# Kernel optimization log

Measured on AMD Instinct MI355X. Metric: run time of the kernel, lower is better.

The kernel has to match this reference:

```python
import jax, jax.numpy as jnp
import numpy as np

N = 100000   # nodes
E = 1600000  # edges (avg degree 16)
F = 128      # num_features
H = 128      # hidden_channels
C = 8        # num_classes


def _gcn_conv(x, src, dst, W, b, num_nodes):
    """PyG GCNConv: add self-loops, symmetric normalization, linear-then-aggregate, +bias."""
    h = x @ W  # [N, out]
    loops = jnp.arange(num_nodes, dtype=src.dtype)
    s = jnp.concatenate([src, loops])
    d = jnp.concatenate([dst, loops])
    deg = jax.ops.segment_sum(jnp.ones_like(s, dtype=h.dtype), d, num_segments=num_nodes)
    dinv = jax.lax.rsqrt(jnp.maximum(deg, 1.0))  # deg >= 1 thanks to self-loops
    norm = dinv[s] * dinv[d]  # [E+N]
    out = jax.ops.segment_sum(h[s] * norm[:, None], d, num_segments=num_nodes)
    return out + b


def setup_inputs() -> dict:
    key = jax.random.key(0)
    k1, k2, k3, k4 = jax.random.split(key, 4)
    x = jax.random.normal(k1, (N, F), dtype=jnp.float32)
    edge_index = jax.random.randint(k2, (2, E), 0, N, dtype=jnp.int32)
    W1 = jax.random.normal(k3, (F, H), dtype=jnp.float32) * (1.0 / np.sqrt(F))
    b1 = jnp.zeros((H,), dtype=jnp.float32)
    W2 = jax.random.normal(k4, (H, C), dtype=jnp.float32) * (1.0 / np.sqrt(H))
    b2 = jnp.zeros((C,), dtype=jnp.float32)
    return {"x": x, "edge_index": edge_index, "W1": W1, "b1": b1, "W2": W2, "b2": b2}


def reference(x, edge_index, W1, b1, W2, b2):
    src, dst = edge_index[0], edge_index[1]
    h = _gcn_conv(x, src, dst, W1, b1, N)
    h = jax.nn.relu(h)
    out = _gcn_conv(h, src, dst, W2, b2, N)
    return out
```

## Files before the change

### kernel.cpp

```cpp
#include <hip/hip_runtime.h>
#include <hip/hip_bf16.h>
#include <hip/hip_fp16.h>

#define NN 100000
#define EE 1600000
#define FF 128
#define HH 128
#define CC 8

#define CH 4096
#define NBK ((NN + 255) / 256)
#define NCH ((EE + CH - 1) / CH)
#define HSZ (NBK * NCH)

typedef _Float16 half8 __attribute__((ext_vector_type(8)));
typedef float f32x4 __attribute__((ext_vector_type(4)));

__global__ __launch_bounds__(1024) void k_scan1(const int* __restrict__ in,
                                                int* __restrict__ outp,
                                                int* __restrict__ bsum, int n) {
  __shared__ int sh[1024];
  int t = threadIdx.x;
  int i = blockIdx.x * 1024 + t;
  int v = (i < n) ? in[i] : 0;
  sh[t] = v;
  __syncthreads();
  for (int offs = 1; offs < 1024; offs <<= 1) {
    int add = (t >= offs) ? sh[t - offs] : 0;
    __syncthreads();
    sh[t] += add;
    __syncthreads();
  }
  if (i < n) outp[i] = sh[t] - v;
  if (t == 1023) bsum[blockIdx.x] = sh[1023];
}

__global__ __launch_bounds__(256) void k_scan2(int* __restrict__ bsum, int nb) {
  __shared__ int sh[256];
  int t = threadIdx.x;
  int v = (t < nb) ? bsum[t] : 0;
  sh[t] = v;
  __syncthreads();
  for (int offs = 1; offs < 256; offs <<= 1) {
    int add = (t >= offs) ? sh[t - offs] : 0;
    __syncthreads();
    sh[t] += add;
    __syncthreads();
  }
  if (t < nb) bsum[t] = sh[t] - v;
}

__global__ __launch_bounds__(1024) void k_scan3(int* __restrict__ outp,
                                                const int* __restrict__ bsum,
                                                int n, int e) {
  int i = blockIdx.x * 1024 + threadIdx.x;
  if (i < n) outp[i] += bsum[blockIdx.x];
  if (i == 0) outp[n] = e;
}

__global__ __launch_bounds__(256) void k_histA(const int* __restrict__ dst,
                                               int* __restrict__ hist) {
  __shared__ int lh[NBK];
  int c = blockIdx.x, t = threadIdx.x;
  for (int b = t; b < NBK; b += 256) lh[b] = 0;
  __syncthreads();
  int e0 = c * CH, e1 = min(e0 + CH, EE);
  for (int j = e0 + t; j < e1; j += 256) atomicAdd(&lh[dst[j] >> 8], 1);
  __syncthreads();
  for (int b = t; b < NBK; b += 256) hist[b * NCH + c] = lh[b];
}

__global__ __launch_bounds__(256) void k_scat_gemm1(
    const int* __restrict__ src, const int* __restrict__ dst,
    const int* __restrict__ hoff, unsigned int* __restrict__ stage,
    const float* __restrict__ x, const float* __restrict__ W,
    __half* __restrict__ h, int n) {
  __shared__ _Float16 Wl[128 * 128];
  int t = threadIdx.x;

  if (blockIdx.x < NCH) {
    int* lcur = (int*)Wl;
    int c = blockIdx.x;
    for (int b = t; b < NBK; b += 256) lcur[b] = hoff[b * NCH + c];
    __syncthreads();
    int e0 = c * CH, e1 = min(e0 + CH, EE);
    for (int j = e0 + t; j < e1; j += 256) {
      int d = dst[j];
      int pos = atomicAdd(&lcur[d >> 8], 1);
      stage[pos] = (unsigned int)src[j] | ((unsigned int)(d & 255) << 17);
    }
    return;
  }

  {
    int c = t & 127;
    int kg0 = t >> 7;
    for (int kg = kg0; kg < 16; kg += 2) {
      _Float16 tmp[8];
#pragma unroll
      for (int j = 0; j < 8; ++j)
        tmp[j] = (_Float16)W[(size_t)(kg * 8 + j) * 128 + c];
      int byteoff = (c * 256 + kg * 16) ^ ((c & 7) << 4);
      *(half8*)((char*)Wl + byteoff) = *(half8*)tmp;
    }
  }
  __syncthreads();

  int row0 = (blockIdx.x - NCH) * 64;
  int w = t >> 6, l = t & 63;
  int rw = w >> 1, cw = w & 1;
  int lr = l & 15, g = l >> 4;

  f32x4 acc[2][4];
#pragma unroll
  for (int ar = 0; ar < 2; ++ar)
#pragma unroll
    for (int bt = 0; bt < 4; ++bt)
#pragma unroll
      for (int r = 0; r < 4; ++r) acc[ar][bt][r] = 0.f;

  for (int kt = 0; kt < 4; ++kt) {
    half8 a[2];
#pragma unroll
    for (int ar = 0; ar < 2; ++ar) {
      int row = row0 + rw * 32 + ar * 16 + lr;
      if (row < n) {
        const float* p = &x[(size_t)row * 128 + kt * 32 + g * 8];
        float4 v0 = *(const float4*)p;
        float4 v1 = *(const float4*)(p + 4);
        a[ar][0] = (_Float16)v0.x; a[ar][1] = (_Float16)v0.y;
        a[ar][2] = (_Float16)v0.z; a[ar][3] = (_Float16)v0.w;
        a[ar][4] = (_Float16)v1.x; a[ar][5] = (_Float16)v1.y;
        a[ar][6] = (_Float16)v1.z; a[ar][7] = (_Float16)v1.w;
      } else {
#pragma unroll
        for (int j = 0; j < 8; ++j) a[ar][j] = (_Float16)0.f;
      }
    }
#pragma unroll
    for (int bt = 0; bt < 4; ++bt) {
      int c = cw * 64 + bt * 16 + lr;
      int byteoff = (c * 256 + kt * 64 + g * 16) ^ ((c & 7) << 4);
      half8 bb = *(const half8*)((const char*)Wl + byteoff);
      acc[0][bt] = __builtin_amdgcn_mfma_f32_16x16x32_f16(a[0], bb, acc[0][bt], 0, 0, 0);
      acc[1][bt] = __builtin_amdgcn_mfma_f32_16x16x32_f16(a[1], bb, acc[1][bt], 0, 0, 0);
    }
  }

#pragma unroll
  for (int ar = 0; ar < 2; ++ar)
#pragma unroll
    for (int bt = 0; bt < 4; ++bt)
#pragma unroll
      for (int r = 0; r < 4; ++r) {
        int row = row0 + rw * 32 + ar * 16 + g * 4 + r;
        int c = cw * 64 + bt * 16 + lr;
        if (row < n) h[(size_t)row * 128 + c] = __float2half(acc[ar][bt][r]);
      }
}

__global__ __launch_bounds__(256) void k_bucketB(const unsigned int* __restrict__ stage,
                                                 const int* __restrict__ hoff,
                                                 int* __restrict__ col,
                                                 int* __restrict__ rowptr,
                                                 float* __restrict__ dinv) {
  __shared__ int lcnt[256];
  __shared__ int lpart[256];
  int b = blockIdx.x, t = threadIdx.x;
  int n0 = b * 256;
  lcnt[t] = 0;
  __syncthreads();
  int e0 = hoff[b * NCH];
  int e1 = hoff[(b + 1) * NCH];
  for (int j = e0 + t; j < e1; j += 256)
    atomicAdd(&lcnt[stage[j] >> 17], 1);
  __syncthreads();
  int c = lcnt[t];
  lpart[t] = c;
  __syncthreads();
  for (int offs = 1; offs < 256; offs <<= 1) {
    int add = (t >= offs) ? lpart[t - offs] : 0;
    __syncthreads();
    lpart[t] += add;
    __syncthreads();
  }
  int base = e0 + lpart[t] - c;
  int node = n0 + t;
  if (node <= NN) rowptr[node] = base;
  if (node < NN) dinv[node] = rsqrtf((float)c + 1.f);
  __syncthreads();
  lcnt[t] = base;
  __syncthreads();
  for (int j = e0 + t; j < e1; j += 256) {
    unsigned int v = stage[j];
    int pos = atomicAdd(&lcnt[v >> 17], 1);
    col[pos] = (int)(v & 0x1FFFFu);
  }
}

__global__ __launch_bounds__(256) void k_agg1(const __half* __restrict__ h,
                                              const int* __restrict__ rowptr,
                                              const int* __restrict__ col,
                                              const float* __restrict__ dinv,
                                              const float* __restrict__ b1,
                                              __half2* __restrict__ out, int n) {
  int wid = threadIdx.x >> 6;
  int lane = threadIdx.x & 63;
  int node = blockIdx.x * 4 + wid;
  if (node >= n) return;
  float dn = dinv[node];
  const __half2* hp = (const __half2*)h;
  float2 acc = make_float2(0.f, 0.f);
  int e0 = rowptr[node], e1 = rowptr[node + 1];
  int e = e0;
  for (; e + 7 < e1; e += 8) {
    int s[8];
#pragma unroll
    for (int u = 0; u < 8; ++u) s[u] = col[e + u];
    float w[8];
    __half2 f[8];
#pragma unroll
    for (int u = 0; u < 8; ++u) w[u] = dinv[s[u]];
#pragma unroll
    for (int u = 0; u < 8; ++u) f[u] = hp[(size_t)s[u] * 64 + lane];
#pragma unroll
    for (int u = 0; u < 8; ++u) {
      float2 ff = __half22float2(f[u]);
      float ww = w[u] * dn;
      acc.x = fmaf(ww, ff.x, acc.x);
      acc.y = fmaf(ww, ff.y, acc.y);
    }
  }
  for (; e + 1 < e1; e += 2) {
    int s0 = col[e], s1 = col[e + 1];
    float w0 = dinv[s0] * dn, w1 = dinv[s1] * dn;
    float2 f0 = __half22float2(hp[(size_t)s0 * 64 + lane]);
    float2 f1 = __half22float2(hp[(size_t)s1 * 64 + lane]);
    acc.x = fmaf(w0, f0.x, acc.x); acc.y = fmaf(w0, f0.y, acc.y);
    acc.x = fmaf(w1, f1.x, acc.x); acc.y = fmaf(w1, f1.y, acc.y);
  }
  if (e < e1) {
    int s = col[e];
    float w = dinv[s] * dn;
    float2 f = __half22float2(hp[(size_t)s * 64 + lane]);
    acc.x = fmaf(w, f.x, acc.x);
    acc.y = fmaf(w, f.y, acc.y);
  }
  {
    float w = dn * dn;
    float2 f = __half22float2(hp[(size_t)node * 64 + lane]);
    acc.x = fmaf(w, f.x, acc.x);
    acc.y = fmaf(w, f.y, acc.y);
  }
  float2 bb = ((const float2*)b1)[lane];
  acc.x = fmaxf(acc.x + bb.x, 0.f);
  acc.y = fmaxf(acc.y + bb.y, 0.f);
  out[(size_t)node * 64 + lane] = __floats2half2_rn(acc.x, acc.y);
}

__global__ __launch_bounds__(256) void k_gemm2(const __half* __restrict__ a,
                                               const float* __restrict__ W2,
                                               __half* __restrict__ h2, int n) {
  int r = blockIdx.x * 256 + threadIdx.x;
  if (r >= n) return;
  float acc[8];
#pragma unroll
  for (int c = 0; c < 8; ++c) acc[c] = 0.f;
  const __half2* ap = (const __half2*)(a + (size_t)r * 128);
#pragma unroll 8
  for (int k2 = 0; k2 < 64; ++k2) {
    float2 v = __half22float2(ap[k2]);
    int k = k2 * 2;
#pragma unroll
    for (int c = 0; c < 8; ++c) {
      acc[c] = fmaf(v.x, W2[(k + 0) * 8 + c], acc[c]);
      acc[c] = fmaf(v.y, W2[(k + 1) * 8 + c], acc[c]);
    }
  }
  union { __half2 h2v[4]; uint4 u; } pk;
#pragma unroll
  for (int c = 0; c < 4; ++c)
    pk.h2v[c] = __floats2half2_rn(acc[2 * c], acc[2 * c + 1]);
  *(uint4*)&h2[(size_t)r * 8] = pk.u;
}

__global__ __launch_bounds__(256) void k_agg2(const __half* __restrict__ h2,
                                              const int* __restrict__ rowptr,
                                              const int* __restrict__ col,
                                              const float* __restrict__ dinv,
                                              const float* __restrict__ b2,
                                              float* __restrict__ out, int n) {
  int gthread = blockIdx.x * 256 + threadIdx.x;
  int node = gthread >> 3, f = gthread & 7;
  if (node >= n) return;
  float dn = dinv[node];
  float acc = 0.f;
  int e0 = rowptr[node], e1 = rowptr[node + 1];
  int e = e0;
  for (; e + 3 < e1; e += 4) {
    int s0 = col[e], s1 = col[e + 1], s2 = col[e + 2], s3 = col[e + 3];
    float w0 = dinv[s0], w1 = dinv[s1], w2 = dinv[s2], w3 = dinv[s3];
    float v0 = __half2float(h2[(size_t)s0 * 8 + f]);
    float v1 = __half2float(h2[(size_t)s1 * 8 + f]);
    float v2 = __half2float(h2[(size_t)s2 * 8 + f]);
    float v3 = __half2float(h2[(size_t)s3 * 8 + f]);
    acc = fmaf(w0 * dn, v0, acc);
    acc = fmaf(w1 * dn, v1, acc);
    acc = fmaf(w2 * dn, v2, acc);
    acc = fmaf(w3 * dn, v3, acc);
  }
  for (; e < e1; ++e) {
    int s = col[e];
    acc = fmaf(dinv[s] * dn, __half2float(h2[(size_t)s * 8 + f]), acc);
  }
  acc = fmaf(dn * dn, __half2float(h2[(size_t)node * 8 + f]), acc);
  out[(size_t)node * 8 + f] = acc + b2[f];
}

extern "C" void kernel_launch(void* const* d_in, const int* in_sizes, int n_in,
                              void* d_out, int out_size, void* d_ws, size_t ws_size,
                              hipStream_t stream) {
  const float* x  = (const float*)d_in[0];
  const int* eidx = (const int*)d_in[1];
  const float* W1 = (const float*)d_in[2];
  const float* b1 = (const float*)d_in[3];
  const float* W2 = (const float*)d_in[4];
  const float* b2 = (const float*)d_in[5];
  float* out = (float*)d_out;
  const int* src = eidx;
  const int* dst = eidx + EE;

  char* ws = (char*)d_ws;
  size_t off = 0;
  auto alloc = [&](size_t bytes) -> char* {
    char* p = ws + off;
    off = (off + bytes + 255) & ~(size_t)255;
    return p;
  };

  float*        dinv   = (float*)       alloc((size_t)NN * 4);
  int*          rowptr = (int*)         alloc((size_t)(NN + 1) * 4);
  int*          bsum   = (int*)         alloc(1024 * 4);
  int*          hist_g = (int*)         alloc((size_t)HSZ * 4);
  int*          hist_s = (int*)         alloc((size_t)(HSZ + 1) * 4);
  unsigned int* stage  = (unsigned int*)alloc((size_t)EE * 4);
  int*          colbuf = (int*)         alloc((size_t)EE * 4);
  __half*       h1     = (__half*)      alloc((size_t)NN * HH * 2);
  __half2*      agg1   = (__half2*)     alloc((size_t)NN * HH * 2);
  __half*       h2     = (__half*)h1;

  int nbScanH = (HSZ + 1023) / 1024;

  k_histA<<<NCH, 256, 0, stream>>>(dst, hist_g);
  k_scan1<<<nbScanH, 1024, 0, stream>>>(hist_g, hist_s, bsum, HSZ);
  k_scan2<<<1, 256, 0, stream>>>(bsum, nbScanH);
  k_scan3<<<nbScanH, 1024, 0, stream>>>(hist_s, bsum, HSZ, EE);

  int nbG1 = (NN + 63) / 64;
  k_scat_gemm1<<<NCH + nbG1, 256, 0, stream>>>(src, dst, hist_s, stage,
                                               x, W1, h1, NN);
  k_bucketB<<<NBK, 256, 0, stream>>>(stage, hist_s, colbuf, rowptr, dinv);

  k_agg1<<<(NN + 3) / 4, 256, 0, stream>>>(h1, rowptr, colbuf, dinv, b1, agg1, NN);
  k_gemm2<<<(NN + 255) / 256, 256, 0, stream>>>((const __half*)agg1, W2, h2, NN);
  k_agg2<<<(NN * 8 + 255) / 256, 256, 0, stream>>>(h2, rowptr, colbuf, dinv,
                                                   b2, out, NN);
}
```

Measured before the change: 165.9 us.

## Fold scan fixup into consumers, stage buckets in LDS, deepen gather unrolls

Drops the k_scan3 launch by having the scatter and bucket kernels add the block-level scan offsets themselves. It doubles the edge chunk size, which halves the histogram size. k_bucketB now copies each bucket's staged edges into shared memory so the second pass avoids re-reading global memory, and falls back to the old path when a bucket holds more than BCAP edges. The gather loops in agg1 and agg2 are unrolled further to keep more loads in flight, at the cost of more registers and possibly lower occupancy.

```diff
diff --git a/kernel.cpp b/kernel.cpp
--- a/kernel.cpp
+++ b/kernel.cpp
@@ -8,10 +8,11 @@
 #define HH 128
 #define CC 8
 
-#define CH 4096
+#define CH 8192
 #define NBK ((NN + 255) / 256)
 #define NCH ((EE + CH - 1) / CH)
 #define HSZ (NBK * NCH)
+#define BCAP 6144
 
 typedef _Float16 half8 __attribute__((ext_vector_type(8)));
 typedef float f32x4 __attribute__((ext_vector_type(4)));
@@ -50,14 +51,6 @@
   if (t < nb) bsum[t] = sh[t] - v;
 }
 
-__global__ __launch_bounds__(1024) void k_scan3(int* __restrict__ outp,
-                                                const int* __restrict__ bsum,
-                                                int n, int e) {
-  int i = blockIdx.x * 1024 + threadIdx.x;
-  if (i < n) outp[i] += bsum[blockIdx.x];
-  if (i == 0) outp[n] = e;
-}
-
 __global__ __launch_bounds__(256) void k_histA(const int* __restrict__ dst,
                                                int* __restrict__ hist) {
   __shared__ int lh[NBK];
@@ -72,7 +65,8 @@
 
 __global__ __launch_bounds__(256) void k_scat_gemm1(
     const int* __restrict__ src, const int* __restrict__ dst,
-    const int* __restrict__ hoff, unsigned int* __restrict__ stage,
+    const int* __restrict__ hist_s, const int* __restrict__ bsum,
+    unsigned int* __restrict__ stage,
     const float* __restrict__ x, const float* __restrict__ W,
     __half* __restrict__ h, int n) {
   __shared__ _Float16 Wl[128 * 128];
@@ -81,7 +75,10 @@
   if (blockIdx.x < NCH) {
     int* lcur = (int*)Wl;
     int c = blockIdx.x;
-    for (int b = t; b < NBK; b += 256) lcur[b] = hoff[b * NCH + c];
+    for (int b = t; b < NBK; b += 256) {
+      int idx = b * NCH + c;
+      lcur[b] = hist_s[idx] + bsum[idx >> 10];
+    }
     __syncthreads();
     int e0 = c * CH, e1 = min(e0 + CH, EE);
     for (int j = e0 + t; j < e1; j += 256) {
@@ -160,20 +157,38 @@
 }
 
 __global__ __launch_bounds__(256) void k_bucketB(const unsigned int* __restrict__ stage,
-                                                 const int* __restrict__ hoff,
+                                                 const int* __restrict__ hist_s,
+                                                 const int* __restrict__ bsum,
                                                  int* __restrict__ col,
                                                  int* __restrict__ rowptr,
                                                  float* __restrict__ dinv) {
+  __shared__ unsigned int sstage[BCAP];
   __shared__ int lcnt[256];
   __shared__ int lpart[256];
   int b = blockIdx.x, t = threadIdx.x;
   int n0 = b * 256;
   lcnt[t] = 0;
-  __syncthreads();
-  int e0 = hoff[b * NCH];
-  int e1 = hoff[(b + 1) * NCH];
-  for (int j = e0 + t; j < e1; j += 256)
-    atomicAdd(&lcnt[stage[j] >> 17], 1);
+  int i0 = b * NCH;
+  int e0 = hist_s[i0] + bsum[i0 >> 10];
+  int e1;
+  if (b == NBK - 1) {
+    e1 = EE;
+  } else {
+    int i1 = (b + 1) * NCH;
+    e1 = hist_s[i1] + bsum[i1 >> 10];
+  }
+  int cnt = e1 - e0;
+  bool lds_path = (cnt <= BCAP);
+  __syncthreads();
+  if (lds_path) {
+    for (int j = t; j < cnt; j += 256) {
+      unsigned int v = stage[e0 + j];
+      sstage[j] = v;
+      atomicAdd(&lcnt[v >> 17], 1);
+    }
+  } else {
+    for (int j = e0 + t; j < e1; j += 256) atomicAdd(&lcnt[stage[j] >> 17], 1);
+  }
   __syncthreads();
   int c = lcnt[t];
   lpart[t] = c;
@@ -191,10 +206,18 @@
   __syncthreads();
   lcnt[t] = base;
   __syncthreads();
-  for (int j = e0 + t; j < e1; j += 256) {
-    unsigned int v = stage[j];
-    int pos = atomicAdd(&lcnt[v >> 17], 1);
-    col[pos] = (int)(v & 0x1FFFFu);
+  if (lds_path) {
+    for (int j = t; j < cnt; j += 256) {
+      unsigned int v = sstage[j];
+      int pos = atomicAdd(&lcnt[v >> 17], 1);
+      col[pos] = (int)(v & 0x1FFFFu);
+    }
+  } else {
+    for (int j = e0 + t; j < e1; j += 256) {
+      unsigned int v = stage[j];
+      int pos = atomicAdd(&lcnt[v >> 17], 1);
+      col[pos] = (int)(v & 0x1FFFFu);
+    }
   }
 }
 
@@ -213,33 +236,43 @@
   float2 acc = make_float2(0.f, 0.f);
   int e0 = rowptr[node], e1 = rowptr[node + 1];
   int e = e0;
-  for (; e + 7 < e1; e += 8) {
-    int s[8];
-#pragma unroll
-    for (int u = 0; u < 8; ++u) s[u] = col[e + u];
-    float w[8];
-    __half2 f[8];
-#pragma unroll
-    for (int u = 0; u < 8; ++u) w[u] = dinv[s[u]];
-#pragma unroll
-    for (int u = 0; u < 8; ++u) f[u] = hp[(size_t)s[u] * 64 + lane];
-#pragma unroll
-    for (int u = 0; u < 8; ++u) {
+  for (; e + 15 < e1; e += 16) {
+    int s[16];
+#pragma unroll
+    for (int u = 0; u < 16; ++u) s[u] = col[e + u];
+    float w[16];
+    __half2 f[16];
+#pragma unroll
+    for (int u = 0; u < 16; ++u) w[u] = dinv[s[u]];
+#pragma unroll
+    for (int u = 0; u < 16; ++u) f[u] = hp[(size_t)s[u] * 64 + lane];
+#pragma unroll
+    for (int u = 0; u < 16; ++u) {
       float2 ff = __half22float2(f[u]);
       float ww = w[u] * dn;
       acc.x = fmaf(ww, ff.x, acc.x);
       acc.y = fmaf(ww, ff.y, acc.y);
     }
   }
-  for (; e + 1 < e1; e += 2) {
-    int s0 = col[e], s1 = col[e + 1];
-    float w0 = dinv[s0] * dn, w1 = dinv[s1] * dn;
-    float2 f0 = __half22float2(hp[(size_t)s0 * 64 + lane]);
-    float2 f1 = __half22float2(hp[(size_t)s1 * 64 + lane]);
-    acc.x = fmaf(w0, f0.x, acc.x); acc.y = fmaf(w0, f0.y, acc.y);
-    acc.x = fmaf(w1, f1.x, acc.x); acc.y = fmaf(w1, f1.y, acc.y);
-  }
-  if (e < e1) {
+  for (; e + 3 < e1; e += 4) {
+    int s[4];
+#pragma unroll
+    for (int u = 0; u < 4; ++u) s[u] = col[e + u];
+    float w[4];
+    __half2 f[4];
+#pragma unroll
+    for (int u = 0; u < 4; ++u) w[u] = dinv[s[u]];
+#pragma unroll
+    for (int u = 0; u < 4; ++u) f[u] = hp[(size_t)s[u] * 64 + lane];
+#pragma unroll
+    for (int u = 0; u < 4; ++u) {
+      float2 ff = __half22float2(f[u]);
+      float ww = w[u] * dn;
+      acc.x = fmaf(ww, ff.x, acc.x);
+      acc.y = fmaf(ww, ff.y, acc.y);
+    }
+  }
+  for (; e < e1; ++e) {
     int s = col[e];
     float w = dinv[s] * dn;
     float2 f = __half22float2(hp[(size_t)s * 64 + lane]);
@@ -297,17 +330,18 @@
   float acc = 0.f;
   int e0 = rowptr[node], e1 = rowptr[node + 1];
   int e = e0;
-  for (; e + 3 < e1; e += 4) {
-    int s0 = col[e], s1 = col[e + 1], s2 = col[e + 2], s3 = col[e + 3];
-    float w0 = dinv[s0], w1 = dinv[s1], w2 = dinv[s2], w3 = dinv[s3];
-    float v0 = __half2float(h2[(size_t)s0 * 8 + f]);
-    float v1 = __half2float(h2[(size_t)s1 * 8 + f]);
-    float v2 = __half2float(h2[(size_t)s2 * 8 + f]);
-    float v3 = __half2float(h2[(size_t)s3 * 8 + f]);
-    acc = fmaf(w0 * dn, v0, acc);
-    acc = fmaf(w1 * dn, v1, acc);
-    acc = fmaf(w2 * dn, v2, acc);
-    acc = fmaf(w3 * dn, v3, acc);
+  for (; e + 7 < e1; e += 8) {
+    int s[8];
+#pragma unroll
+    for (int u = 0; u < 8; ++u) s[u] = col[e + u];
+    float w[8];
+    float v[8];
+#pragma unroll
+    for (int u = 0; u < 8; ++u) w[u] = dinv[s[u]];
+#pragma unroll
+    for (int u = 0; u < 8; ++u) v[u] = __half2float(h2[(size_t)s[u] * 8 + f]);
+#pragma unroll
+    for (int u = 0; u < 8; ++u) acc = fmaf(w[u] * dn, v[u], acc);
   }
   for (; e < e1; ++e) {
     int s = col[e];
@@ -342,7 +376,7 @@
   int*          rowptr = (int*)         alloc((size_t)(NN + 1) * 4);
   int*          bsum   = (int*)         alloc(1024 * 4);
   int*          hist_g = (int*)         alloc((size_t)HSZ * 4);
-  int*          hist_s = (int*)         alloc((size_t)(HSZ + 1) * 4);
+  int*          hist_s = (int*)         alloc((size_t)HSZ * 4);
   unsigned int* stage  = (unsigned int*)alloc((size_t)EE * 4);
   int*          colbuf = (int*)         alloc((size_t)EE * 4);
   __half*       h1     = (__half*)      alloc((size_t)NN * HH * 2);
@@ -354,12 +388,11 @@
   k_histA<<<NCH, 256, 0, stream>>>(dst, hist_g);
   k_scan1<<<nbScanH, 1024, 0, stream>>>(hist_g, hist_s, bsum, HSZ);
   k_scan2<<<1, 256, 0, stream>>>(bsum, nbScanH);
-  k_scan3<<<nbScanH, 1024, 0, stream>>>(hist_s, bsum, HSZ, EE);
 
   int nbG1 = (NN + 63) / 64;
-  k_scat_gemm1<<<NCH + nbG1, 256, 0, stream>>>(src, dst, hist_s, stage,
+  k_scat_gemm1<<<NCH + nbG1, 256, 0, stream>>>(src, dst, hist_s, bsum, stage,
                                                x, W1, h1, NN);
-  k_bucketB<<<NBK, 256, 0, stream>>>(stage, hist_s, colbuf, rowptr, dinv);
+  k_bucketB<<<NBK, 256, 0, stream>>>(stage, hist_s, bsum, colbuf, rowptr, dinv);
 
   k_agg1<<<(NN + 3) / 4, 256, 0, stream>>>(h1, rowptr, colbuf, dinv, b1, agg1, NN);
   k_gemm2<<<(NN + 255) / 256, 256, 0, stream>>>((const __half*)agg1, W2, h2, NN);
```

New measurement: 175.7 us. +5.9%, slower.
